# Kernel tuning notes

Hardware: AMD Instinct MI355X
Metric: run time of the kernel (lower is better)

The kernel has to match this reference:

```python
import jax, jax.numpy as jnp
import numpy as np

N_HEADS = 16

def setup_inputs() -> dict:
    key = jax.random.key(0)
    ks = jax.random.split(key, 6)
    B, S, D = 2, 2048, 1024
    sc = 0.02
    return {
        "x": jax.random.normal(ks[0], (B, S, D), dtype=jnp.float32),
        "Wq": jax.random.normal(ks[1], (D, D), dtype=jnp.float32) * sc,
        "Wk": jax.random.normal(ks[2], (D, D), dtype=jnp.float32) * sc,
        "Wv": jax.random.normal(ks[3], (D, D), dtype=jnp.float32) * sc,
        "Wo": jax.random.normal(ks[4], (D, D), dtype=jnp.float32) * sc,
        "bo": jnp.zeros((D,), dtype=jnp.float32),
        "stride": 64,
    }

def _strided_mask(S: int, stride: int):
    # local window |i-j|<=1  OR  |i-j| == k*stride (k>=1); diff==0 is in the window
    i = jnp.arange(S)[:, None]
    j = jnp.arange(S)[None, :]
    diff = jnp.abs(i - j)
    return (diff <= 1) | (diff % stride == 0)  # [S, S] bool

def reference(x, Wq, Wk, Wv, Wo, bo, stride):
    B, S, D = x.shape
    H = N_HEADS
    Dh = D // H
    # q/k/v projections: nn.Linear(bias=False) applies x @ W.T
    def proj(W):
        return (x @ W.T).reshape(B, S, H, Dh).transpose(0, 2, 1, 3)  # [B,H,S,Dh]
    q, k, v = proj(Wq), proj(Wk), proj(Wv)
    scores = jnp.einsum('bhqd,bhkd->bhqk', q, k) / jnp.sqrt(jnp.float32(Dh))
    mask = _strided_mask(S, stride)  # [S,S]
    scores = jnp.where(mask[None, None], scores, -jnp.inf)
    attn = jax.nn.softmax(scores, axis=-1)  # dropout is identity in eval
    out = jnp.einsum('bhqk,bhkd->bhqd', attn, v)  # [B,H,S,Dh]
    out = out.transpose(0, 2, 1, 3).reshape(B, S, D)
    return out @ Wo.T + bo
```

## Files before the change

### kernel.cpp

```cpp
#include <hip/hip_runtime.h>
#include <hip/hip_bf16.h>


typedef __bf16 bf16;
typedef __attribute__((ext_vector_type(4))) __bf16 bf16x4;
typedef __attribute__((ext_vector_type(8))) __bf16 bf16x8;
typedef __attribute__((ext_vector_type(4))) float f32x4;
typedef __attribute__((ext_vector_type(4))) unsigned int u32x4;

constexpr int S_ = 2048;
constexpr int D_ = 1024;
constexpr int H_ = 16;
constexpr int DH = 64;
constexpr int M_ = 2 * S_;

__device__ __forceinline__ void gload_lds16(const bf16* g, bf16* l) {
    __builtin_amdgcn_global_load_lds(
        (const __attribute__((address_space(1))) void*)g,
        (__attribute__((address_space(3))) void*)l, 16, 0, 0);
}

#define BARRIER_FULL() do { asm volatile("" ::: "memory"); \
    __builtin_amdgcn_sched_barrier(0); \
    __builtin_amdgcn_s_barrier(); \
    __builtin_amdgcn_sched_barrier(0); \
    asm volatile("" ::: "memory"); } while (0)

#define WAIT_LGKM0() do { asm volatile("s_waitcnt lgkmcnt(0)" ::: "memory"); \
    __builtin_amdgcn_sched_barrier(0); } while (0)

#define WAIT_VM0() do { asm volatile("s_waitcnt vmcnt(0)" ::: "memory"); \
    __builtin_amdgcn_sched_barrier(0); } while (0)

#define WAIT_VM4() do { asm volatile("s_waitcnt vmcnt(4)" ::: "memory"); \
    __builtin_amdgcn_sched_barrier(0); } while (0)

#define SCHED_FENCE() __builtin_amdgcn_sched_barrier(0)

__device__ __forceinline__ void stage32(const bf16* __restrict__ G, int base_row,
                                        int kcol, bf16* lds, int wave, int lane)
{
    const int rIn = lane >> 2;
    const int g   = (lane & 3) ^ ((lane >> 2) & 3) ^ (lane >> 4);
    #pragma unroll
    for (int l = 0; l < 2; ++l) {
        const int R = (wave * 2 + l) * 16;
        gload_lds16(G + (size_t)(base_row + R + rIn) * D_ + kcol + g * 8,
                    lds + R * 32);
    }
}

__global__ __launch_bounds__(512, 1)
void gemm_qkv_p2(const bf16* __restrict__ A,
                 const bf16* __restrict__ W,
                 bf16* __restrict__ C)
{
    constexpr int BK = 32;
    constexpr int NT = D_ / BK;
    constexpr int TSLOT = 256 * BK;
    __shared__ __align__(16) bf16 As[3 * TSLOT];
    __shared__ __align__(16) bf16 Bs[3 * TSLOT];

    const int tid  = threadIdx.x;
    const int wave = tid >> 6;
    const int lane = tid & 63;
    const int wm = wave >> 2;
    const int wn = wave & 3;

    const int lid = blockIdx.y * 12 + blockIdx.x;
    const int xcd = lid & 7, pos = lid >> 3;
    const int bxs = (xcd & 1) * 6 + pos % 6;
    const int bys = (xcd >> 1) * 4 + pos / 6;
    const int bm = bys * 256;
    const int bn = bxs * 256;

    const int l15 = lane & 15;
    const int rs  = (lane >> 4) ^ (lane & 3) ^ ((lane >> 2) & 3);
    const int aRd = wm * 4096 + l15 * 32 + rs * 8;
    const int bRd = wn * 2048 + l15 * 32 + rs * 8;

    f32x4 acc[8][4];
    #pragma unroll
    for (int i = 0; i < 8; ++i)
        #pragma unroll
        for (int j = 0; j < 4; ++j) acc[i][j] = f32x4{0.f, 0.f, 0.f, 0.f};

    bf16x8 aF0[4], aF1[4], bF[4];

#define MFMA16(AF, HH) do { _Pragma("unroll") \
    for (int fm = 0; fm < 4; ++fm) { _Pragma("unroll") \
        for (int fn = 0; fn < 4; ++fn) \
            acc[(HH) * 4 + fm][fn] = __builtin_amdgcn_mfma_f32_16x16x32_bf16( \
                AF[fm], bF[fn], acc[(HH) * 4 + fm][fn], 0, 0, 0); \
    } } while (0)

    stage32(A, bm, 0,  As,         wave, lane);
    stage32(W, bn, 0,  Bs,         wave, lane);
    stage32(A, bm, BK, As + TSLOT, wave, lane);
    stage32(W, bn, BK, Bs + TSLOT, wave, lane);
    WAIT_VM4();
    BARRIER_FULL();

    int cur = 0;
    for (int t = 0; t < NT; ++t) {
        const int ss = (cur + 2 >= 3) ? (cur - 1) : (cur + 2);
        const bf16* aslot = As + cur * TSLOT;
        const bf16* bslot = Bs + cur * TSLOT;
        const bool pre = (t + 2) < NT;
        const int kn = (t + 2) * BK;

        #pragma unroll
        for (int fn = 0; fn < 4; ++fn)
            bF[fn] = *(const bf16x8*)(bslot + bRd + fn * 512);
        #pragma unroll
        for (int fm = 0; fm < 4; ++fm)
            aF0[fm] = *(const bf16x8*)(aslot + aRd + fm * 512);
        if (pre) stage32(A, bm, kn, As + ss * TSLOT, wave, lane);
        BARRIER_FULL(); WAIT_LGKM0();
        #pragma unroll
        for (int fm = 0; fm < 4; ++fm)
            aF1[fm] = *(const bf16x8*)(aslot + aRd + 2048 + fm * 512);
        SCHED_FENCE();
        __builtin_amdgcn_s_setprio(1); MFMA16(aF0, 0); __builtin_amdgcn_s_setprio(0);
        BARRIER_FULL();

        if (pre) stage32(W, bn, kn, Bs + ss * TSLOT, wave, lane);
        BARRIER_FULL(); WAIT_LGKM0();
        __builtin_amdgcn_s_setprio(1); MFMA16(aF1, 1); __builtin_amdgcn_s_setprio(0);
        if (pre) { WAIT_VM4(); } else { WAIT_VM0(); }
        BARRIER_FULL();

        cur = (cur + 1 >= 3) ? 0 : (cur + 1);
    }
#undef MFMA16

    #pragma unroll
    for (int fm8 = 0; fm8 < 8; ++fm8) {
        #pragma unroll
        for (int fn4 = 0; fn4 < 4; ++fn4) {
            const int n = bn + wn * 64 + fn4 * 16 + l15;
            const int z = n >> 10, col = n & 1023;
            bf16* Cz = C + (size_t)z * M_ * D_;
            const int mb = bm + wm * 128 + fm8 * 16 + (lane >> 4) * 4;
            #pragma unroll
            for (int r2 = 0; r2 < 4; ++r2)
                Cz[(size_t)(mb + r2) * D_ + col] = (bf16)acc[fm8][fn4][r2];
        }
    }
}

__device__ __forceinline__ void stage64(const bf16* __restrict__ G, int base_row,
                                        int kcol, bf16* lds, int wave, int lane)
{
    const int rIn = lane >> 3;
    const int g   = (lane & 7) ^ rIn;
    #pragma unroll
    for (int l = 0; l < 2; ++l) {
        const int c = wave * 2 + l;
        gload_lds16(G + (size_t)(base_row + c * 8 + rIn) * D_ + kcol + g * 8,
                    lds + c * 512);
    }
}

__global__ __launch_bounds__(512, 1)
void gemm_o_2ph(const bf16* __restrict__ A,
                const bf16* __restrict__ W,
                float* __restrict__ Cf,
                const float* __restrict__ bias)
{
    constexpr int BK = 64;
    constexpr int NT = D_ / BK;
    constexpr int TSLOT = 128 * BK;
    __shared__ __align__(16) bf16 As[3 * TSLOT];
    __shared__ __align__(16) bf16 Bs[3 * TSLOT];

    const int tid  = threadIdx.x;
    const int wave = tid >> 6;
    const int lane = tid & 63;
    const int wm = wave >> 2;
    const int wn = wave & 3;

    const int lid = blockIdx.y * 8 + blockIdx.x;
    const int xcd = lid & 7, pos = lid >> 3;
    const int bxs = (xcd & 3) * 2 + (pos & 1);
    const int bys = (xcd >> 2) * 16 + (pos >> 1);
    const int bm = bys * 128;
    const int bn = bxs * 128;

    const int l15 = lane & 15;
    const int hi  = lane >> 4;
    const int r7  = l15 & 7;

    int aOff[2][4], bOff[2][2];
    #pragma unroll
    for (int ks = 0; ks < 2; ++ks) {
        #pragma unroll
        for (int fm = 0; fm < 4; ++fm)
            aOff[ks][fm] = (wm * 64 + fm * 16 + l15) * 64 + (((ks * 4 + hi) ^ r7) * 8);
        #pragma unroll
        for (int fn = 0; fn < 2; ++fn)
            bOff[ks][fn] = (wn * 32 + fn * 16 + l15) * 64 + (((ks * 4 + hi) ^ r7) * 8);
    }

    f32x4 acc[4][2];
    #pragma unroll
    for (int i = 0; i < 4; ++i)
        #pragma unroll
        for (int j = 0; j < 2; ++j) acc[i][j] = f32x4{0.f, 0.f, 0.f, 0.f};

    bf16x8 aF0[4], aF1[4], bF[2][2];

    stage64(A, bm, 0,  As,         wave, lane);
    stage64(W, bn, 0,  Bs,         wave, lane);
    stage64(A, bm, BK, As + TSLOT, wave, lane);
    stage64(W, bn, BK, Bs + TSLOT, wave, lane);
    WAIT_VM4();
    BARRIER_FULL();

    int cur = 0;
    for (int t = 0; t < NT; ++t) {
        const int ss = (cur + 2 >= 3) ? (cur - 1) : (cur + 2);
        const bf16* aslot = As + cur * TSLOT;
        const bf16* bslot = Bs + cur * TSLOT;
        const bool pre = (t + 2) < NT;
        const int kn = (t + 2) * BK;

        #pragma unroll
        for (int ks = 0; ks < 2; ++ks)
            #pragma unroll
            for (int fn = 0; fn < 2; ++fn)
                bF[ks][fn] = *(const bf16x8*)(bslot + bOff[ks][fn]);
        #pragma unroll
        for (int fm = 0; fm < 4; ++fm)
            aF0[fm] = *(const bf16x8*)(aslot + aOff[0][fm]);
        if (pre) stage64(A, bm, kn, As + ss * TSLOT, wave, lane);
        BARRIER_FULL(); WAIT_LGKM0();
        __builtin_amdgcn_s_setprio(1);
        #pragma unroll
        for (int fm = 0; fm < 4; ++fm)
            #pragma unroll
            for (int fn = 0; fn < 2; ++fn)
                acc[fm][fn] = __builtin_amdgcn_mfma_f32_16x16x32_bf16(
                    aF0[fm], bF[0][fn], acc[fm][fn], 0, 0, 0);
        __builtin_amdgcn_s_setprio(0);
        BARRIER_FULL();

        #pragma unroll
        for (int fm = 0; fm < 4; ++fm)
            aF1[fm] = *(const bf16x8*)(aslot + aOff[1][fm]);
        if (pre) stage64(W, bn, kn, Bs + ss * TSLOT, wave, lane);
        BARRIER_FULL(); WAIT_LGKM0();
        __builtin_amdgcn_s_setprio(1);
        #pragma unroll
        for (int fm = 0; fm < 4; ++fm)
            #pragma unroll
            for (int fn = 0; fn < 2; ++fn)
                acc[fm][fn] = __builtin_amdgcn_mfma_f32_16x16x32_bf16(
                    aF1[fm], bF[1][fn], acc[fm][fn], 0, 0, 0);
        __builtin_amdgcn_s_setprio(0);
        if (pre) { WAIT_VM4(); } else { WAIT_VM0(); }
        BARRIER_FULL();
        cur = (cur + 1 >= 3) ? 0 : (cur + 1);
    }

    #pragma unroll
    for (int fm = 0; fm < 4; ++fm) {
        #pragma unroll
        for (int fn = 0; fn < 2; ++fn) {
            const int n = bn + wn * 32 + fn * 16 + l15;
            const float bv = bias[n];
            const int mb = bm + wm * 64 + fm * 16 + hi * 4;
            #pragma unroll
            for (int r2 = 0; r2 < 4; ++r2)
                Cf[(size_t)(mb + r2) * D_ + n] = acc[fm][fn][r2] + bv;
        }
    }
}

template<bool AF32, bool BF32, bool CF32, bool BIAS>
__global__ __launch_bounds__(256)
void gemm_bt(const void* __restrict__ Av,
             const void* __restrict__ W0v, const void* __restrict__ W1v,
             const void* __restrict__ W2v,
             void* __restrict__ Cv, const float* __restrict__ bias)
{
    constexpr int BM = 128, BK = 64;
    constexpr int N = D_, K = D_;
    __shared__ __align__(16) bf16 As[BM * BK];
    __shared__ __align__(16) bf16 Bs[BM * BK];

    const int z = blockIdx.z;
    const void* Wv_ = (z == 0) ? W0v : (z == 1) ? W1v : W2v;

    const int tid  = threadIdx.x;
    const int wave = tid >> 6;
    const int lane = tid & 63;

    const int bm = blockIdx.y * BM;
    const int bn = blockIdx.x * BM;
    const int wr = wave >> 1;
    const int wc = wave & 1;

    f32x4 acc[4][4];
    #pragma unroll
    for (int i = 0; i < 4; ++i)
        #pragma unroll
        for (int j = 0; j < 4; ++j)
            acc[i][j] = f32x4{0.f, 0.f, 0.f, 0.f};

    const int ldRow = lane >> 3;
    const int ldCol = (lane & 7) * 8;

    for (int kt = 0; kt < K; kt += BK) {
        if (AF32) {
            const float* A = (const float*)Av;
            #pragma unroll
            for (int it = 0; it < 8; ++it) {
                const int flat = (it * 256 + tid) * 4;
                const int row = flat >> 6, col = flat & 63;
                const float4 v = *(const float4*)(A + (size_t)(bm + row) * K + kt + col);
                bf16x4 p = { (bf16)v.x, (bf16)v.y, (bf16)v.z, (bf16)v.w };
                *(bf16x4*)&As[row * BK + col] = p;
            }
        } else {
            const bf16* A = (const bf16*)Av;
            #pragma unroll
            for (int q = 0; q < 4; ++q) {
                const int c = wave * 4 + q;
                const int row = c * 8 + ldRow;
                gload_lds16(A + (size_t)(bm + row) * K + kt + ldCol, &As[c * 8 * BK]);
            }
        }
        if (BF32) {
            const float* W = (const float*)Wv_;
            #pragma unroll
            for (int it = 0; it < 8; ++it) {
                const int flat = (it * 256 + tid) * 4;
                const int row = flat >> 6, col = flat & 63;
                const float4 v = *(const float4*)(W + (size_t)(bn + row) * K + kt + col);
                bf16x4 p = { (bf16)v.x, (bf16)v.y, (bf16)v.z, (bf16)v.w };
                *(bf16x4*)&Bs[row * BK + col] = p;
            }
        } else {
            const bf16* W = (const bf16*)Wv_;
            #pragma unroll
            for (int q = 0; q < 4; ++q) {
                const int c = wave * 4 + q;
                const int row = c * 8 + ldRow;
                gload_lds16(W + (size_t)(bn + row) * K + kt + ldCol, &Bs[c * 8 * BK]);
            }
        }
        __syncthreads();
        #pragma unroll
        for (int kk = 0; kk < 2; ++kk) {
            const int k0 = kk * 32 + (lane >> 4) * 8;
            bf16x8 af[4], bfv[4];
            #pragma unroll
            for (int mi = 0; mi < 4; ++mi)
                af[mi] = *(const bf16x8*)&As[(wr * 64 + mi * 16 + (lane & 15)) * BK + k0];
            #pragma unroll
            for (int ni = 0; ni < 4; ++ni)
                bfv[ni] = *(const bf16x8*)&Bs[(wc * 64 + ni * 16 + (lane & 15)) * BK + k0];
            #pragma unroll
            for (int mi = 0; mi < 4; ++mi)
                #pragma unroll
                for (int ni = 0; ni < 4; ++ni)
                    acc[mi][ni] = __builtin_amdgcn_mfma_f32_16x16x32_bf16(
                        af[mi], bfv[ni], acc[mi][ni], 0, 0, 0);
        }
        __syncthreads();
    }

    #pragma unroll
    for (int mi = 0; mi < 4; ++mi) {
        #pragma unroll
        for (int ni = 0; ni < 4; ++ni) {
            const int n  = bn + wc * 64 + ni * 16 + (lane & 15);
            const int mb = bm + wr * 64 + mi * 16 + (lane >> 4) * 4;
            float bv = 0.f;
            if (BIAS) bv = bias[n];
            #pragma unroll
            for (int r2 = 0; r2 < 4; ++r2) {
                const int m = mb + r2;
                if (CF32) {
                    ((float*)Cv)[(size_t)m * N + n] = acc[mi][ni][r2] + bv;
                } else {
                    bf16* Cc = (bf16*)Cv + (size_t)z * M_ * D_;
                    Cc[(size_t)m * N + n] = (bf16)(acc[mi][ni][r2] + bv);
                }
            }
        }
    }
}

__global__ __launch_bounds__(256)
void convert_to_bf16(const float* __restrict__ x,
                     const float* __restrict__ w0, const float* __restrict__ w1,
                     const float* __restrict__ w2, const float* __restrict__ w3,
                     bf16* __restrict__ out)
{
    const size_t eid = ((size_t)blockIdx.x * 256 + threadIdx.x) * 8;
    const float* src; size_t off;
    if (eid < (size_t)(1u << 22)) { src = x; off = eid; }
    else {
        const size_t t = eid - (1u << 22);
        const int k = (int)(t >> 20);
        off = t & ((1u << 20) - 1);
        src = (k == 0) ? w0 : (k == 1) ? w1 : (k == 2) ? w2 : w3;
    }
    const float4 a = *(const float4*)(src + off);
    const float4 c = *(const float4*)(src + off + 4);
    bf16x8 v = { (bf16)a.x, (bf16)a.y, (bf16)a.z, (bf16)a.w,
                 (bf16)c.x, (bf16)c.y, (bf16)c.z, (bf16)c.w };
    *(bf16x8*)(out + eid) = v;
}

__device__ __forceinline__ unsigned pk2bf(float lo, float hi) {
    const unsigned a = __builtin_bit_cast(unsigned short, (bf16)lo);
    const unsigned b = __builtin_bit_cast(unsigned short, (bf16)hi);
    return a | (b << 16);
}

__global__ __launch_bounds__(256)
void attn_mfma(bf16* __restrict__ QA, const bf16* __restrict__ Kw,
               const bf16* __restrict__ Vw)
{
    const int lane = threadIdx.x & 63;
    const int wid  = blockIdx.x * 4 + (threadIdx.x >> 6);
    const int r = wid & 63;
    const int h = (wid >> 6) & (H_ - 1);
    const int b = wid >> 10;

    const int qlo = lane & 15;
    const int g   = lane >> 4;
    const size_t rb = (size_t)b * S_;
    const int col0 = h * DH;
    const float scale = 0.125f;

    f32x4 accS[2][2];
    #pragma unroll
    for (int a = 0; a < 2; ++a)
        #pragma unroll
        for (int c = 0; c < 2; ++c) accS[a][c] = f32x4{0.f,0.f,0.f,0.f};

    #pragma unroll
    for (int c = 0; c < 2; ++c) {
        bf16x8 kf[2], qf[2];
        #pragma unroll
        for (int t = 0; t < 2; ++t) {
            const size_t row = rb + (size_t)(r + 64 * (t * 16 + qlo));
            kf[t] = *(const bf16x8*)&Kw[row * D_ + col0 + c * 32 + g * 8];
            qf[t] = *(const bf16x8*)&QA[row * D_ + col0 + c * 32 + g * 8];
        }
        #pragma unroll
        for (int kt = 0; kt < 2; ++kt)
            #pragma unroll
            for (int qt = 0; qt < 2; ++qt)
                accS[kt][qt] = __builtin_amdgcn_mfma_f32_16x16x32_bf16(
                    kf[kt], qf[qt], accS[kt][qt], 0, 0, 0);
    }

    const int s_nb = lane & 31;
    const int side = lane >> 5;
    const int i_nb = r + 64 * s_nb;
    const int j_nb = side ? (i_nb + 1) : (i_nb - 1);
    const bool nbv = (unsigned)j_nb < (unsigned)S_;
    const int j_sf = nbv ? j_nb : i_nb;
    float nbd = 0.f;
    #pragma unroll
    for (int t = 0; t < 8; ++t) {
        const bf16x8 qv = *(const bf16x8*)&QA[(rb + i_nb) * D_ + col0 + t * 8];
        const bf16x8 kv = *(const bf16x8*)&Kw[(rb + j_sf) * D_ + col0 + t * 8];
        #pragma unroll
        for (int e = 0; e < 8; ++e) nbd += (float)qv[e] * (float)kv[e];
    }
    const float NEGINF = -__builtin_inff();
    float nb = nbv ? nbd * scale : NEGINF;

    float mx[2] = { NEGINF, NEGINF };
    #pragma unroll
    for (int kt = 0; kt < 2; ++kt)
        #pragma unroll
        for (int qt = 0; qt < 2; ++qt)
            #pragma unroll
            for (int rr = 0; rr < 4; ++rr)
                mx[qt] = fmaxf(mx[qt], accS[kt][qt][rr]);
    mx[0] *= scale; mx[1] *= scale;
    mx[g & 1] = fmaxf(mx[g & 1], nb);
    #pragma unroll
    for (int x = 16; x <= 32; x <<= 1) {
        mx[0] = fmaxf(mx[0], __shfl_xor(mx[0], x));
        mx[1] = fmaxf(mx[1], __shfl_xor(mx[1], x));
    }
    float p[2][2][4];
    float sm[2] = { 0.f, 0.f };
    #pragma unroll
    for (int kt = 0; kt < 2; ++kt)
        #pragma unroll
        for (int qt = 0; qt < 2; ++qt)
            #pragma unroll
            for (int rr = 0; rr < 4; ++rr) {
                const float e = __expf(accS[kt][qt][rr] * scale - mx[qt]);
                p[kt][qt][rr] = e;
                sm[qt] += e;
            }
    float nbp = __expf(nb - mx[g & 1]);
    sm[g & 1] += nbp;
    #pragma unroll
    for (int x = 16; x <= 32; x <<= 1) {
        sm[0] += __shfl_xor(sm[0], x);
        sm[1] += __shfl_xor(sm[1], x);
    }
    const float inv[2] = { 1.f / sm[0], 1.f / sm[1] };
    #pragma unroll
    for (int kt = 0; kt < 2; ++kt)
        #pragma unroll
        for (int qt = 0; qt < 2; ++qt)
            #pragma unroll
            for (int rr = 0; rr < 4; ++rr) p[kt][qt][rr] *= inv[qt];
    nbp *= inv[g & 1];

    unsigned pk_[2][2][2];
    #pragma unroll
    for (int qt = 0; qt < 2; ++qt)
        #pragma unroll
        for (int kt = 0; kt < 2; ++kt)
            #pragma unroll
            for (int w = 0; w < 2; ++w)
                pk_[qt][kt][w] = pk2bf(p[kt][qt][2 * w], p[kt][qt][2 * w + 1]);

    const int srcA = qlo + 32 * (g & 1);
    const int srcB = srcA + 16;
    const int kts  = g >> 1;
    bf16x8 pa[2];
    #pragma unroll
    for (int qt = 0; qt < 2; ++qt) {
        u32x4 fr;
        #pragma unroll
        for (int w = 0; w < 2; ++w) {
            const unsigned a0 = (unsigned)__shfl((int)pk_[qt][0][w], srcA);
            const unsigned a1 = (unsigned)__shfl((int)pk_[qt][1][w], srcA);
            fr[w] = kts ? a1 : a0;
            const unsigned b0 = (unsigned)__shfl((int)pk_[qt][0][w], srcB);
            const unsigned b1 = (unsigned)__shfl((int)pk_[qt][1][w], srcB);
            fr[2 + w] = kts ? b1 : b0;
        }
        pa[qt] = __builtin_bit_cast(bf16x8, fr);
    }

    f32x4 accO[2][4];
    #pragma unroll
    for (int qt = 0; qt < 2; ++qt)
        #pragma unroll
        for (int dt = 0; dt < 4; ++dt) accO[qt][dt] = f32x4{0.f,0.f,0.f,0.f};
    #pragma unroll
    for (int dt = 0; dt < 4; ++dt) {
        bf16x8 vf;
        #pragma unroll
        for (int e = 0; e < 8; ++e)
            vf[e] = Vw[(rb + (size_t)(r + 64 * (g * 8 + e))) * D_ + col0 + dt * 16 + qlo];
        accO[0][dt] = __builtin_amdgcn_mfma_f32_16x16x32_bf16(pa[0], vf, accO[0][dt], 0, 0, 0);
        accO[1][dt] = __builtin_amdgcn_mfma_f32_16x16x32_bf16(pa[1], vf, accO[1][dt], 0, 0, 0);
    }

    #pragma unroll
    for (int qt = 0; qt < 2; ++qt)
        #pragma unroll
        for (int rr = 0; rr < 4; ++rr) {
            const int q  = qt * 16 + g * 4 + rr;
            const int iq = r + 64 * q;
            const float pm = __shfl(nbp, q);
            const float pp = __shfl(nbp, q + 32);
            const int jm = iq > 0 ? iq - 1 : 0;
            const int jp = iq < S_ - 1 ? iq + 1 : S_ - 1;
            #pragma unroll
            for (int dt = 0; dt < 4; ++dt) {
                const int d = col0 + dt * 16 + qlo;
                const float vm = (float)Vw[(rb + jm) * D_ + d];
                const float vp = (float)Vw[(rb + jp) * D_ + d];
                const float o = accO[qt][dt][rr] + pm * vm + pp * vp;
                QA[(rb + iq) * D_ + d] = (bf16)o;
            }
        }
}

extern "C" void kernel_launch(void* const* d_in, const int* in_sizes, int n_in,
                              void* d_out, int out_size, void* d_ws, size_t ws_size,
                              hipStream_t stream)
{
    const float* x  = (const float*)d_in[0];
    const float* Wq = (const float*)d_in[1];
    const float* Wk = (const float*)d_in[2];
    const float* Wv = (const float*)d_in[3];
    const float* Wo = (const float*)d_in[4];
    const float* bo = (const float*)d_in[5];

    bf16* qws = (bf16*)d_ws;
    bf16* kws = qws + (size_t)M_ * D_;
    bf16* vws = kws + (size_t)M_ * D_;

    const bool fast = ws_size >= (size_t)40 * 1024 * 1024;

    if (fast) {
        bf16* xb  = vws + (size_t)M_ * D_;
        bf16* wqb = xb + (1u << 22);
        bf16* wob = wqb + 3 * (1u << 20);

        convert_to_bf16<<<4096, 256, 0, stream>>>(x, Wq, Wk, Wv, Wo, xb);

        gemm_qkv_p2<<<dim3(3 * D_ / 256, M_ / 256), 512, 0, stream>>>(xb, wqb, qws);

        attn_mfma<<<dim3(2 * H_ * 64 / 4), 256, 0, stream>>>(qws, kws, vws);

        gemm_o_2ph<<<dim3(D_ / 128, M_ / 128), 512, 0, stream>>>(
            qws, wob, (float*)d_out, bo);
    } else {
        gemm_bt<true, true, false, false><<<dim3(D_/128, M_/128, 3), 256, 0, stream>>>(
            x, Wq, Wk, Wv, qws, nullptr);

        attn_mfma<<<dim3(2 * H_ * 64 / 4), 256, 0, stream>>>(qws, kws, vws);

        gemm_bt<false, true, true, true><<<dim3(D_/128, M_/128, 1), 256, 0, stream>>>(
            qws, Wo, nullptr, nullptr, (float*)d_out, bo);
    }
}
```

Measured before the change: 90.52 us.

## Replace 256x256 QKV GEMM tiling with shared 128x128 BK=64 body

The QKV projection GEMM no longer uses its own 256x256-tile, BK=32 kernel. It now runs the same 128x128, BK=64 templated body as the output projection, with the epilogue selected by a template flag. This launches four times as many blocks (768 instead of 192), which should fill the 256 CUs better and reduce tail imbalance. In exchange, each block does more global/LDS traffic per FLOP because each tile reuses less data.

```diff
diff --git a/kernel.cpp b/kernel.cpp
--- a/kernel.cpp
+++ b/kernel.cpp
@@ -35,69 +35,60 @@
 #define WAIT_VM4() do { asm volatile("s_waitcnt vmcnt(4)" ::: "memory"); \
     __builtin_amdgcn_sched_barrier(0); } while (0)
 
-#define SCHED_FENCE() __builtin_amdgcn_sched_barrier(0)
-
-__device__ __forceinline__ void stage32(const bf16* __restrict__ G, int base_row,
+__device__ __forceinline__ void stage64(const bf16* __restrict__ G, int base_row,
                                         int kcol, bf16* lds, int wave, int lane)
 {
-    const int rIn = lane >> 2;
-    const int g   = (lane & 3) ^ ((lane >> 2) & 3) ^ (lane >> 4);
+    const int rIn = lane >> 3;
+    const int g   = (lane & 7) ^ rIn;
     #pragma unroll
     for (int l = 0; l < 2; ++l) {
-        const int R = (wave * 2 + l) * 16;
-        gload_lds16(G + (size_t)(base_row + R + rIn) * D_ + kcol + g * 8,
-                    lds + R * 32);
-    }
-}
-
-__global__ __launch_bounds__(512, 1)
-void gemm_qkv_p2(const bf16* __restrict__ A,
-                 const bf16* __restrict__ W,
-                 bf16* __restrict__ C)
-{
-    constexpr int BK = 32;
+        const int c = wave * 2 + l;
+        gload_lds16(G + (size_t)(base_row + c * 8 + rIn) * D_ + kcol + g * 8,
+                    lds + c * 512);
+    }
+}
+
+template<bool OUT_BF16>
+__device__ __forceinline__ void gemm128_body(
+    const bf16* __restrict__ A, const bf16* __restrict__ W,
+    void* __restrict__ Cv, const float* __restrict__ bias,
+    int bm, int bn, int wave, int lane)
+{
+    constexpr int BK = 64;
     constexpr int NT = D_ / BK;
-    constexpr int TSLOT = 256 * BK;
+    constexpr int TSLOT = 128 * BK;
     __shared__ __align__(16) bf16 As[3 * TSLOT];
     __shared__ __align__(16) bf16 Bs[3 * TSLOT];
 
-    const int tid  = threadIdx.x;
-    const int wave = tid >> 6;
-    const int lane = tid & 63;
     const int wm = wave >> 2;
     const int wn = wave & 3;
-
-    const int lid = blockIdx.y * 12 + blockIdx.x;
-    const int xcd = lid & 7, pos = lid >> 3;
-    const int bxs = (xcd & 1) * 6 + pos % 6;
-    const int bys = (xcd >> 1) * 4 + pos / 6;
-    const int bm = bys * 256;
-    const int bn = bxs * 256;
-
     const int l15 = lane & 15;
-    const int rs  = (lane >> 4) ^ (lane & 3) ^ ((lane >> 2) & 3);
-    const int aRd = wm * 4096 + l15 * 32 + rs * 8;
-    const int bRd = wn * 2048 + l15 * 32 + rs * 8;
-
-    f32x4 acc[8][4];
-    #pragma unroll
-    for (int i = 0; i < 8; ++i)
-        #pragma unroll
-        for (int j = 0; j < 4; ++j) acc[i][j] = f32x4{0.f, 0.f, 0.f, 0.f};
-
-    bf16x8 aF0[4], aF1[4], bF[4];
-
-#define MFMA16(AF, HH) do { _Pragma("unroll") \
-    for (int fm = 0; fm < 4; ++fm) { _Pragma("unroll") \
-        for (int fn = 0; fn < 4; ++fn) \
-            acc[(HH) * 4 + fm][fn] = __builtin_amdgcn_mfma_f32_16x16x32_bf16( \
-                AF[fm], bF[fn], acc[(HH) * 4 + fm][fn], 0, 0, 0); \
-    } } while (0)
-
-    stage32(A, bm, 0,  As,         wave, lane);
-    stage32(W, bn, 0,  Bs,         wave, lane);
-    stage32(A, bm, BK, As + TSLOT, wave, lane);
-    stage32(W, bn, BK, Bs + TSLOT, wave, lane);
+    const int hi  = lane >> 4;
+    const int r7  = l15 & 7;
+
+    int aOff[2][4], bOff[2][2];
+    #pragma unroll
+    for (int ks = 0; ks < 2; ++ks) {
+        #pragma unroll
+        for (int fm = 0; fm < 4; ++fm)
+            aOff[ks][fm] = (wm * 64 + fm * 16 + l15) * 64 + (((ks * 4 + hi) ^ r7) * 8);
+        #pragma unroll
+        for (int fn = 0; fn < 2; ++fn)
+            bOff[ks][fn] = (wn * 32 + fn * 16 + l15) * 64 + (((ks * 4 + hi) ^ r7) * 8);
+    }
+
+    f32x4 acc[4][2];
+    #pragma unroll
+    for (int i = 0; i < 4; ++i)
+        #pragma unroll
+        for (int j = 0; j < 2; ++j) acc[i][j] = f32x4{0.f, 0.f, 0.f, 0.f};
+
+    bf16x8 aF0[4], aF1[4], bF[2][2];
+
+    stage64(A, bm, 0,  As,         wave, lane);
+    stage64(W, bn, 0,  Bs,         wave, lane);
+    stage64(A, bm, BK, As + TSLOT, wave, lane);
+    stage64(W, bn, BK, Bs + TSLOT, wave, lane);
     WAIT_VM4();
     BARRIER_FULL();
 
@@ -110,122 +101,6 @@
         const int kn = (t + 2) * BK;
 
         #pragma unroll
-        for (int fn = 0; fn < 4; ++fn)
-            bF[fn] = *(const bf16x8*)(bslot + bRd + fn * 512);
-        #pragma unroll
-        for (int fm = 0; fm < 4; ++fm)
-            aF0[fm] = *(const bf16x8*)(aslot + aRd + fm * 512);
-        if (pre) stage32(A, bm, kn, As + ss * TSLOT, wave, lane);
-        BARRIER_FULL(); WAIT_LGKM0();
-        #pragma unroll
-        for (int fm = 0; fm < 4; ++fm)
-            aF1[fm] = *(const bf16x8*)(aslot + aRd + 2048 + fm * 512);
-        SCHED_FENCE();
-        __builtin_amdgcn_s_setprio(1); MFMA16(aF0, 0); __builtin_amdgcn_s_setprio(0);
-        BARRIER_FULL();
-
-        if (pre) stage32(W, bn, kn, Bs + ss * TSLOT, wave, lane);
-        BARRIER_FULL(); WAIT_LGKM0();
-        __builtin_amdgcn_s_setprio(1); MFMA16(aF1, 1); __builtin_amdgcn_s_setprio(0);
-        if (pre) { WAIT_VM4(); } else { WAIT_VM0(); }
-        BARRIER_FULL();
-
-        cur = (cur + 1 >= 3) ? 0 : (cur + 1);
-    }
-#undef MFMA16
-
-    #pragma unroll
-    for (int fm8 = 0; fm8 < 8; ++fm8) {
-        #pragma unroll
-        for (int fn4 = 0; fn4 < 4; ++fn4) {
-            const int n = bn + wn * 64 + fn4 * 16 + l15;
-            const int z = n >> 10, col = n & 1023;
-            bf16* Cz = C + (size_t)z * M_ * D_;
-            const int mb = bm + wm * 128 + fm8 * 16 + (lane >> 4) * 4;
-            #pragma unroll
-            for (int r2 = 0; r2 < 4; ++r2)
-                Cz[(size_t)(mb + r2) * D_ + col] = (bf16)acc[fm8][fn4][r2];
-        }
-    }
-}
-
-__device__ __forceinline__ void stage64(const bf16* __restrict__ G, int base_row,
-                                        int kcol, bf16* lds, int wave, int lane)
-{
-    const int rIn = lane >> 3;
-    const int g   = (lane & 7) ^ rIn;
-    #pragma unroll
-    for (int l = 0; l < 2; ++l) {
-        const int c = wave * 2 + l;
-        gload_lds16(G + (size_t)(base_row + c * 8 + rIn) * D_ + kcol + g * 8,
-                    lds + c * 512);
-    }
-}
-
-__global__ __launch_bounds__(512, 1)
-void gemm_o_2ph(const bf16* __restrict__ A,
-                const bf16* __restrict__ W,
-                float* __restrict__ Cf,
-                const float* __restrict__ bias)
-{
-    constexpr int BK = 64;
-    constexpr int NT = D_ / BK;
-    constexpr int TSLOT = 128 * BK;
-    __shared__ __align__(16) bf16 As[3 * TSLOT];
-    __shared__ __align__(16) bf16 Bs[3 * TSLOT];
-
-    const int tid  = threadIdx.x;
-    const int wave = tid >> 6;
-    const int lane = tid & 63;
-    const int wm = wave >> 2;
-    const int wn = wave & 3;
-
-    const int lid = blockIdx.y * 8 + blockIdx.x;
-    const int xcd = lid & 7, pos = lid >> 3;
-    const int bxs = (xcd & 3) * 2 + (pos & 1);
-    const int bys = (xcd >> 2) * 16 + (pos >> 1);
-    const int bm = bys * 128;
-    const int bn = bxs * 128;
-
-    const int l15 = lane & 15;
-    const int hi  = lane >> 4;
-    const int r7  = l15 & 7;
-
-    int aOff[2][4], bOff[2][2];
-    #pragma unroll
-    for (int ks = 0; ks < 2; ++ks) {
-        #pragma unroll
-        for (int fm = 0; fm < 4; ++fm)
-            aOff[ks][fm] = (wm * 64 + fm * 16 + l15) * 64 + (((ks * 4 + hi) ^ r7) * 8);
-        #pragma unroll
-        for (int fn = 0; fn < 2; ++fn)
-            bOff[ks][fn] = (wn * 32 + fn * 16 + l15) * 64 + (((ks * 4 + hi) ^ r7) * 8);
-    }
-
-    f32x4 acc[4][2];
-    #pragma unroll
-    for (int i = 0; i < 4; ++i)
-        #pragma unroll
-        for (int j = 0; j < 2; ++j) acc[i][j] = f32x4{0.f, 0.f, 0.f, 0.f};
-
-    bf16x8 aF0[4], aF1[4], bF[2][2];
-
-    stage64(A, bm, 0,  As,         wave, lane);
-    stage64(W, bn, 0,  Bs,         wave, lane);
-    stage64(A, bm, BK, As + TSLOT, wave, lane);
-    stage64(W, bn, BK, Bs + TSLOT, wave, lane);
-    WAIT_VM4();
-    BARRIER_FULL();
-
-    int cur = 0;
-    for (int t = 0; t < NT; ++t) {
-        const int ss = (cur + 2 >= 3) ? (cur - 1) : (cur + 2);
-        const bf16* aslot = As + cur * TSLOT;
-        const bf16* bslot = Bs + cur * TSLOT;
-        const bool pre = (t + 2) < NT;
-        const int kn = (t + 2) * BK;
-
-        #pragma unroll
         for (int ks = 0; ks < 2; ++ks)
             #pragma unroll
             for (int fn = 0; fn < 2; ++fn)
@@ -268,13 +143,50 @@
         #pragma unroll
         for (int fn = 0; fn < 2; ++fn) {
             const int n = bn + wn * 32 + fn * 16 + l15;
-            const float bv = bias[n];
             const int mb = bm + wm * 64 + fm * 16 + hi * 4;
-            #pragma unroll
-            for (int r2 = 0; r2 < 4; ++r2)
-                Cf[(size_t)(mb + r2) * D_ + n] = acc[fm][fn][r2] + bv;
-        }
-    }
+            if (OUT_BF16) {
+                bf16* Cz = (bf16*)Cv + (size_t)(n >> 10) * M_ * D_;
+                const int col = n & 1023;
+                #pragma unroll
+                for (int r2 = 0; r2 < 4; ++r2)
+                    Cz[(size_t)(mb + r2) * D_ + col] = (bf16)acc[fm][fn][r2];
+            } else {
+                const float bv = bias[n];
+                #pragma unroll
+                for (int r2 = 0; r2 < 4; ++r2)
+                    ((float*)Cv)[(size_t)(mb + r2) * D_ + n] = acc[fm][fn][r2] + bv;
+            }
+        }
+    }
+}
+
+__global__ __launch_bounds__(512, 1)
+void gemm_qkv_128(const bf16* __restrict__ A,
+                  const bf16* __restrict__ W,
+                  bf16* __restrict__ C)
+{
+    const int wave = threadIdx.x >> 6;
+    const int lane = threadIdx.x & 63;
+    const int lid = blockIdx.y * 24 + blockIdx.x;
+    const int xcd = lid & 7, pos = lid >> 3;
+    const int bxs = (xcd & 1) * 12 + pos % 12;
+    const int bys = (xcd >> 1) * 8 + pos / 12;
+    gemm128_body<true>(A, W, C, nullptr, bys * 128, bxs * 128, wave, lane);
+}
+
+__global__ __launch_bounds__(512, 1)
+void gemm_o_2ph(const bf16* __restrict__ A,
+                const bf16* __restrict__ W,
+                float* __restrict__ Cf,
+                const float* __restrict__ bias)
+{
+    const int wave = threadIdx.x >> 6;
+    const int lane = threadIdx.x & 63;
+    const int lid = blockIdx.y * 8 + blockIdx.x;
+    const int xcd = lid & 7, pos = lid >> 3;
+    const int bxs = (xcd & 3) * 2 + (pos & 1);
+    const int bys = (xcd >> 2) * 16 + (pos >> 1);
+    gemm128_body<false>(A, W, Cf, bias, bys * 128, bxs * 128, wave, lane);
 }
 
 template<bool AF32, bool BF32, bool CF32, bool BIAS>
@@ -608,7 +520,7 @@
 
         convert_to_bf16<<<4096, 256, 0, stream>>>(x, Wq, Wk, Wv, Wo, xb);
 
-        gemm_qkv_p2<<<dim3(3 * D_ / 256, M_ / 256), 512, 0, stream>>>(xb, wqb, qws);
+        gemm_qkv_128<<<dim3(3 * D_ / 128, M_ / 128), 512, 0, stream>>>(xb, wqb, qws);
 
         attn_mfma<<<dim3(2 * H_ * 64 / 4), 256, 0, stream>>>(qws, kws, vws);
 
```

Measured after the change: 93.10 us. 2.9% more time.

## Restructure QKV GEMM into BK=64 quarter-tile pipeline with double-buffered halves

Applied to the files above, without the earlier changes.

Rewrites the fused QKV projection GEMM so each 256x256 tile is split into 128-row halves in LDS, with K-steps of 64 and double buffering instead of a triple buffer with K-steps of 32. Each iteration now runs four quarter-tile MFMA phases, and each phase's staging of the next halves is interleaved with compute on the current ones. The goal is to halve the number of loop iterations and barriers per element and to keep global-to-LDS loads overlapped with MFMA work. In exchange the schedule is more intricate, holds more fragment registers, and could hit a buffer hazard if the staging order is wrong.

```diff
diff --git a/kernel.cpp b/kernel.cpp
--- a/kernel.cpp
+++ b/kernel.cpp
@@ -35,31 +35,29 @@
 #define WAIT_VM4() do { asm volatile("s_waitcnt vmcnt(4)" ::: "memory"); \
     __builtin_amdgcn_sched_barrier(0); } while (0)
 
-#define SCHED_FENCE() __builtin_amdgcn_sched_barrier(0)
-
-__device__ __forceinline__ void stage32(const bf16* __restrict__ G, int base_row,
+__device__ __forceinline__ void stage64(const bf16* __restrict__ G, int base_row,
                                         int kcol, bf16* lds, int wave, int lane)
 {
-    const int rIn = lane >> 2;
-    const int g   = (lane & 3) ^ ((lane >> 2) & 3) ^ (lane >> 4);
+    const int rIn = lane >> 3;
+    const int g   = (lane & 7) ^ rIn;
     #pragma unroll
     for (int l = 0; l < 2; ++l) {
-        const int R = (wave * 2 + l) * 16;
-        gload_lds16(G + (size_t)(base_row + R + rIn) * D_ + kcol + g * 8,
-                    lds + R * 32);
+        const int c = wave * 2 + l;
+        gload_lds16(G + (size_t)(base_row + c * 8 + rIn) * D_ + kcol + g * 8,
+                    lds + c * 512);
     }
 }
 
 __global__ __launch_bounds__(512, 1)
-void gemm_qkv_p2(const bf16* __restrict__ A,
+void gemm_qkv_8p(const bf16* __restrict__ A,
                  const bf16* __restrict__ W,
                  bf16* __restrict__ C)
 {
-    constexpr int BK = 32;
+    constexpr int BK = 64;
     constexpr int NT = D_ / BK;
-    constexpr int TSLOT = 256 * BK;
-    __shared__ __align__(16) bf16 As[3 * TSLOT];
-    __shared__ __align__(16) bf16 Bs[3 * TSLOT];
+    constexpr int HS = 128 * BK;
+    __shared__ __align__(16) bf16 As[2][2][HS];
+    __shared__ __align__(16) bf16 Bs[2][2][HS];
 
     const int tid  = threadIdx.x;
     const int wave = tid >> 6;
@@ -75,9 +73,27 @@
     const int bn = bxs * 256;
 
     const int l15 = lane & 15;
-    const int rs  = (lane >> 4) ^ (lane & 3) ^ ((lane >> 2) & 3);
-    const int aRd = wm * 4096 + l15 * 32 + rs * 8;
-    const int bRd = wn * 2048 + l15 * 32 + rs * 8;
+    const int hi  = lane >> 4;
+    const int r7  = l15 & 7;
+    const int bh  = wn >> 1;
+
+    int aOff[2][4][2], bOff[2][2][2];
+    #pragma unroll
+    for (int mh = 0; mh < 2; ++mh)
+        #pragma unroll
+        for (int fm = 0; fm < 4; ++fm)
+            #pragma unroll
+            for (int kk = 0; kk < 2; ++kk)
+                aOff[mh][fm][kk] = (mh * 64 + fm * 16 + l15) * 64
+                                 + (((kk * 4 + hi) ^ r7) * 8);
+    #pragma unroll
+    for (int nh = 0; nh < 2; ++nh)
+        #pragma unroll
+        for (int fn = 0; fn < 2; ++fn)
+            #pragma unroll
+            for (int kk = 0; kk < 2; ++kk)
+                bOff[nh][fn][kk] = ((wn & 1) * 64 + nh * 32 + fn * 16 + l15) * 64
+                                 + (((kk * 4 + hi) ^ r7) * 8);
 
     f32x4 acc[8][4];
     #pragma unroll
@@ -85,80 +101,87 @@
         #pragma unroll
         for (int j = 0; j < 4; ++j) acc[i][j] = f32x4{0.f, 0.f, 0.f, 0.f};
 
-    bf16x8 aF0[4], aF1[4], bF[4];
-
-#define MFMA16(AF, HH) do { _Pragma("unroll") \
+    bf16x8 aF[4][2], bF0[2][2], bF1[2][2];
+
+#define Q16(MH, NH, BF) do { _Pragma("unroll") \
     for (int fm = 0; fm < 4; ++fm) { _Pragma("unroll") \
-        for (int fn = 0; fn < 4; ++fn) \
-            acc[(HH) * 4 + fm][fn] = __builtin_amdgcn_mfma_f32_16x16x32_bf16( \
-                AF[fm], bF[fn], acc[(HH) * 4 + fm][fn], 0, 0, 0); \
-    } } while (0)
-
-    stage32(A, bm, 0,  As,         wave, lane);
-    stage32(W, bn, 0,  Bs,         wave, lane);
-    stage32(A, bm, BK, As + TSLOT, wave, lane);
-    stage32(W, bn, BK, Bs + TSLOT, wave, lane);
+        for (int fn = 0; fn < 2; ++fn) { _Pragma("unroll") \
+            for (int kk = 0; kk < 2; ++kk) \
+                acc[(MH)*4+fm][(NH)*2+fn] = __builtin_amdgcn_mfma_f32_16x16x32_bf16( \
+                    aF[fm][kk], BF[fn][kk], acc[(MH)*4+fm][(NH)*2+fn], 0, 0, 0); \
+    } } } while (0)
+
+    stage64(A, bm +   0, 0,  &As[0][0][0], wave, lane);
+    stage64(A, bm + 128, 0,  &As[0][1][0], wave, lane);
+    stage64(W, bn +   0, 0,  &Bs[0][0][0], wave, lane);
+    stage64(W, bn + 128, 0,  &Bs[0][1][0], wave, lane);
+    stage64(W, bn +   0, BK, &Bs[1][0][0], wave, lane);
+    stage64(A, bm +   0, BK, &As[1][0][0], wave, lane);
     WAIT_VM4();
     BARRIER_FULL();
 
-    int cur = 0;
     for (int t = 0; t < NT; ++t) {
-        const int ss = (cur + 2 >= 3) ? (cur - 1) : (cur + 2);
-        const bf16* aslot = As + cur * TSLOT;
-        const bf16* bslot = Bs + cur * TSLOT;
-        const bool pre = (t + 2) < NT;
-        const int kn = (t + 2) * BK;
-
-        #pragma unroll
-        for (int fn = 0; fn < 4; ++fn)
-            bF[fn] = *(const bf16x8*)(bslot + bRd + fn * 512);
-        #pragma unroll
-        for (int fm = 0; fm < 4; ++fm)
-            aF0[fm] = *(const bf16x8*)(aslot + aRd + fm * 512);
-        if (pre) stage32(A, bm, kn, As + ss * TSLOT, wave, lane);
+        const int d = t & 1;
+        const bf16* aH = &As[d][wm][0];
+        const bf16* bH = &Bs[d][bh][0];
+        const bool pre1 = (t + 1) < NT;
+        const bool pre2 = (t + 2) < NT;
+        const int k1 = (t + 1) * BK, k2 = (t + 2) * BK;
+
+        #pragma unroll
+        for (int fn = 0; fn < 2; ++fn)
+            #pragma unroll
+            for (int kk = 0; kk < 2; ++kk)
+                bF0[fn][kk] = *(const bf16x8*)(bH + bOff[0][fn][kk]);
+        #pragma unroll
+        for (int fm = 0; fm < 4; ++fm)
+            #pragma unroll
+            for (int kk = 0; kk < 2; ++kk)
+                aF[fm][kk] = *(const bf16x8*)(aH + aOff[0][fm][kk]);
+        if (pre1) stage64(A, bm + 128, k1, &As[d ^ 1][1][0], wave, lane);
         BARRIER_FULL(); WAIT_LGKM0();
-        #pragma unroll
-        for (int fm = 0; fm < 4; ++fm)
-            aF1[fm] = *(const bf16x8*)(aslot + aRd + 2048 + fm * 512);
-        SCHED_FENCE();
-        __builtin_amdgcn_s_setprio(1); MFMA16(aF0, 0); __builtin_amdgcn_s_setprio(0);
+        __builtin_amdgcn_s_setprio(1); Q16(0, 0, bF0); __builtin_amdgcn_s_setprio(0);
         BARRIER_FULL();
 
-        if (pre) stage32(W, bn, kn, Bs + ss * TSLOT, wave, lane);
+        #pragma unroll
+        for (int fn = 0; fn < 2; ++fn)
+            #pragma unroll
+            for (int kk = 0; kk < 2; ++kk)
+                bF1[fn][kk] = *(const bf16x8*)(bH + bOff[1][fn][kk]);
+        if (pre1) stage64(W, bn + 128, k1, &Bs[d ^ 1][1][0], wave, lane);
         BARRIER_FULL(); WAIT_LGKM0();
-        __builtin_amdgcn_s_setprio(1); MFMA16(aF1, 1); __builtin_amdgcn_s_setprio(0);
-        if (pre) { WAIT_VM4(); } else { WAIT_VM0(); }
+        __builtin_amdgcn_s_setprio(1); Q16(0, 1, bF1); __builtin_amdgcn_s_setprio(0);
         BARRIER_FULL();
 
-        cur = (cur + 1 >= 3) ? 0 : (cur + 1);
-    }
-#undef MFMA16
-
-    #pragma unroll
-    for (int fm8 = 0; fm8 < 8; ++fm8) {
-        #pragma unroll
-        for (int fn4 = 0; fn4 < 4; ++fn4) {
-            const int n = bn + wn * 64 + fn4 * 16 + l15;
-            const int z = n >> 10, col = n & 1023;
-            bf16* Cz = C + (size_t)z * M_ * D_;
-            const int mb = bm + wm * 128 + fm8 * 16 + (lane >> 4) * 4;
+        #pragma unroll
+        for (int fm = 0; fm < 4; ++fm)
+            #pragma unroll
+            for (int kk = 0; kk < 2; ++kk)
+                aF[fm][kk] = *(const bf16x8*)(aH + aOff[1][fm][kk]);
+        if (pre2) stage64(W, bn + 0, k2, &Bs[d][0][0], wave, lane);
+        BARRIER_FULL(); WAIT_LGKM0();
+        __builtin_amdgcn_s_setprio(1); Q16(1, 1, bF1); __builtin_amdgcn_s_setprio(0);
+        BARRIER_FULL();
+
+        if (pre2) stage64(A, bm + 0, k2, &As[d][0][0], wave, lane);
+        __builtin_amdgcn_s_setprio(1); Q16(1, 0, bF0); __builtin_amdgcn_s_setprio(0);
+        if (pre2) { WAIT_VM4(); } else { WAIT_VM0(); }
+        BARRIER_FULL();
+    }
+#undef Q16
+
+    #pragma unroll
+    for (int i = 0; i < 8; ++i) {
+        #pragma unroll
+        for (int j = 0; j < 4; ++j) {
+            const int n = bn + wn * 64 + j * 16 + l15;
+            bf16* Cz = C + (size_t)(n >> 10) * M_ * D_;
+            const int col = n & 1023;
+            const int mb = bm + wm * 128 + i * 16 + hi * 4;
             #pragma unroll
             for (int r2 = 0; r2 < 4; ++r2)
-                Cz[(size_t)(mb + r2) * D_ + col] = (bf16)acc[fm8][fn4][r2];
-        }
-    }
-}
-
-__device__ __forceinline__ void stage64(const bf16* __restrict__ G, int base_row,
-                                        int kcol, bf16* lds, int wave, int lane)
-{
-    const int rIn = lane >> 3;
-    const int g   = (lane & 7) ^ rIn;
-    #pragma unroll
-    for (int l = 0; l < 2; ++l) {
-        const int c = wave * 2 + l;
-        gload_lds16(G + (size_t)(base_row + c * 8 + rIn) * D_ + kcol + g * 8,
-                    lds + c * 512);
+                Cz[(size_t)(mb + r2) * D_ + col] = (bf16)acc[i][j][r2];
+        }
     }
 }
 
@@ -608,7 +631,7 @@
 
         convert_to_bf16<<<4096, 256, 0, stream>>>(x, Wq, Wk, Wv, Wo, xb);
 
-        gemm_qkv_p2<<<dim3(3 * D_ / 256, M_ / 256), 512, 0, stream>>>(xb, wqb, qws);
+        gemm_qkv_8p<<<dim3(3 * D_ / 256, M_ / 256), 512, 0, stream>>>(xb, wqb, qws);
 
         attn_mfma<<<dim3(2 * H_ * 64 / 4), 256, 0, stream>>>(qws, kws, vws);
 
```

Measured after the change: 85.83 us. -5.2%, faster.
